# Performance work log

Hardware: AMD Instinct MI355X
Metric: run time of the kernel (lower is better)

The kernel has to match this reference:

```python
import jax, jax.numpy as jnp
import numpy as np

N = 100000
E = 1600000
NFEAT, NHID, NCLASS = 602, 128, 41
EPS = 1e-5


def _spmm(rows, cols, vals, h):
    # out[r] = sum_{e: rows[e]==r} vals[e] * h[cols[e]]
    return jax.ops.segment_sum(vals[:, None] * h[cols], rows, num_segments=N)


def _layernorm(h, g, b):
    mu = jnp.mean(h, axis=-1, keepdims=True)
    var = jnp.var(h, axis=-1, keepdims=True)
    return (h - mu) * jax.lax.rsqrt(var + EPS) * g + b


def setup_inputs() -> dict:
    key = jax.random.key(0)
    ks = jax.random.split(key, 12)
    x = jax.random.normal(ks[0], (N, NFEAT), dtype=jnp.float32)
    rows = jax.random.randint(ks[1], (3, E), 0, N, dtype=jnp.int32)
    cols = jax.random.randint(ks[2], (3, E), 0, N, dtype=jnp.int32)
    # normalized-adjacency-like edge weights (~1/avg_degree scale)
    vals = jax.random.uniform(ks[3], (3, E), dtype=jnp.float32) / 16.0
    W1 = jax.random.normal(ks[4], (NFEAT, NHID), dtype=jnp.float32) / np.sqrt(NFEAT)
    b1 = jnp.zeros((NHID,), dtype=jnp.float32)
    W2 = jax.random.normal(ks[5], (NHID, NHID), dtype=jnp.float32) / np.sqrt(NHID)
    b2 = jnp.zeros((NHID,), dtype=jnp.float32)
    W3 = jax.random.normal(ks[6], (NHID, NHID), dtype=jnp.float32) / np.sqrt(NHID)
    b3 = jnp.zeros((NHID,), dtype=jnp.float32)
    ln_g = jnp.ones((NHID,), dtype=jnp.float32)
    ln_b = jnp.zeros((NHID,), dtype=jnp.float32)
    Wout = jax.random.normal(ks[7], (NHID, NCLASS), dtype=jnp.float32) / np.sqrt(NHID)
    bout = jnp.zeros((NCLASS,), dtype=jnp.float32)
    return {"x": x, "rows": rows, "cols": cols, "vals": vals,
            "W1": W1, "b1": b1, "W2": W2, "b2": b2, "W3": W3, "b3": b3,
            "ln_g": ln_g, "ln_b": ln_b, "Wout": Wout, "bout": bout}


def reference(x, rows, cols, vals, W1, b1, W2, b2, W3, b3, ln_g, ln_b, Wout, bout):
    # gc1: spmm(adj0, x @ W1) + b1 -> shared LayerNorm -> ReLU (dropout = eval identity)
    h = _spmm(rows[0], cols[0], vals[0], x @ W1) + b1
    h = jax.nn.relu(_layernorm(h, ln_g, ln_b))
    # gc2 with adj1
    h = _spmm(rows[1], cols[1], vals[1], h @ W2) + b2
    h = jax.nn.relu(_layernorm(h, ln_g, ln_b))
    # gc3 with adj2
    h = _spmm(rows[2], cols[2], vals[2], h @ W3) + b3
    h = jax.nn.relu(_layernorm(h, ln_g, ln_b))
    logits = h @ Wout + bout
    return jax.nn.log_softmax(logits, axis=1)
```

## Files before the change

kernel.cpp:

```cpp
#include <hip/hip_runtime.h>
#include <cstddef>

#define N_NODES 100000
#define E_EDGES 1600000
#define NFEAT   602
#define NHID    128
#define NCLASS  41
#define LN_EPS  1e-5f

typedef __bf16 bf16x8 __attribute__((ext_vector_type(8)));
typedef float f32x4 __attribute__((ext_vector_type(4)));
typedef unsigned short ushort8 __attribute__((ext_vector_type(8)));
typedef int intx4 __attribute__((ext_vector_type(4)));
typedef float fltx4 __attribute__((ext_vector_type(4)));

__device__ inline float bflo(unsigned int u) {
    return __builtin_bit_cast(float, u << 16);
}
__device__ inline float bfhi(unsigned int u) {
    return __builtin_bit_cast(float, u & 0xFFFF0000u);
}
__device__ inline unsigned short f2bf(float f) {
    return __builtin_bit_cast(unsigned short, (__bf16)f);
}

#define NT1 19
#define NT2 4

__global__ __launch_bounds__(256) void k_prep_all(
    const float* __restrict__ W1, const float* __restrict__ W2,
    const float* __restrict__ W3, unsigned short* __restrict__ Wf1,
    unsigned short* __restrict__ Wf2, unsigned short* __restrict__ Wf3)
{
    const int wid = (blockIdx.x * 256 + threadIdx.x) >> 6;
    const int lane = threadIdx.x & 63;
    const float* W; unsigned short* Wf; int K; int lw;
    if (wid < NT1 * 8)            { W = W1; Wf = Wf1; K = NFEAT; lw = wid; }
    else if (wid < (NT1 + NT2) * 8) { W = W2; Wf = Wf2; K = NHID; lw = wid - NT1 * 8; }
    else if (wid < (NT1 + 2 * NT2) * 8) { W = W3; Wf = Wf3; K = NHID; lw = wid - (NT1 + NT2) * 8; }
    else return;
    const int t = lw >> 3, n = lw & 7;
    const int fr = lane & 15, kh = lane >> 4;
    const int c = n * 16 + fr;
    ushort8 v;
#pragma unroll
    for (int j = 0; j < 8; ++j) {
        int k = t * 32 + kh * 8 + j;
        float x = (k < K) ? W[(size_t)k * 128 + c] : 0.f;
        v[j] = f2bf(x);
    }
    *reinterpret_cast<ushort8*>(Wf + ((size_t)lw * 64 + lane) * 8) = v;
}

template<int KK, bool BF16A>
__global__ __launch_bounds__(512) void k_gemm_slab(
    const void* __restrict__ Ain, const unsigned short* __restrict__ Wfrag,
    unsigned short* __restrict__ C, int M)
{
    constexpr int NT = (KK + 31) / 32;
    constexpr int KPAD = ((KK + 7) / 8) * 8 + 8;
    __shared__ unsigned short As[64 * KPAD + 8];

    const int tid = threadIdx.x;
    const int row0 = blockIdx.x * 64;
    const int nrow = (M - row0 < 64) ? (M - row0) : 64;
    const int total = nrow * KK;

    if (!BF16A) {
        const float* A32 = (const float*)Ain + (size_t)row0 * KK;
        constexpr int totalFull = 64 * KK;
#pragma unroll 4
        for (int base = 0; base < totalFull; base += 2048) {
            int i = base + tid * 4;
            if (i < totalFull) {
                float4 v = make_float4(0.f, 0.f, 0.f, 0.f);
                if (i + 4 <= total) {
                    v = *reinterpret_cast<const float4*>(A32 + i);
                } else if (i < total) {
                    float tmp[4] = {0.f, 0.f, 0.f, 0.f};
#pragma unroll
                    for (int e = 0; e < 4; ++e) if (i + e < total) tmp[e] = A32[i + e];
                    v = make_float4(tmp[0], tmp[1], tmp[2], tmp[3]);
                }
                int row = i / KK;
                int col = i - row * KK;
                unsigned int d0 = (unsigned int)f2bf(v.x) | ((unsigned int)f2bf(v.y) << 16);
                unsigned int d1 = (unsigned int)f2bf(v.z) | ((unsigned int)f2bf(v.w) << 16);
                int a0 = row * KPAD + col;
                int a1 = (col == KK - 2) ? (row + 1) * KPAD : a0 + 2;
                *reinterpret_cast<unsigned int*>(&As[a0]) = d0;
                *reinterpret_cast<unsigned int*>(&As[a1]) = d1;
            }
        }
    } else {
        const unsigned short* A16 = (const unsigned short*)Ain + (size_t)row0 * KK;
        constexpr int totalFull = 64 * KK;
#pragma unroll
        for (int base = 0; base < totalFull; base += 4096) {
            int i = base + tid * 8;
            if (i < totalFull) {
                ushort8 v;
#pragma unroll
                for (int j = 0; j < 8; ++j) v[j] = 0;
                if (i + 8 <= total) v = *reinterpret_cast<const ushort8*>(A16 + i);
                int row = i / KK;
                int col = i - row * KK;
                *reinterpret_cast<ushort8*>(&As[row * KPAD + col]) = v;
            }
        }
    }
    __syncthreads();

    const int wv = tid >> 6, lane = tid & 63;
    const int fr = lane & 15, kh = lane >> 4;
    const int mfr = wv >> 1;
    const int ch = wv & 1;
    const unsigned short* abase = &As[(mfr * 16 + fr) * KPAD + kh * 8];
    const unsigned short* wbase = Wfrag + ((size_t)(ch * 4) * 64 + lane) * 8;

    f32x4 acc[4];
#pragma unroll
    for (int n = 0; n < 4; ++n) acc[n] = (f32x4)(0.f);

    bf16x8 bcur[4];
#pragma unroll
    for (int n = 0; n < 4; ++n)
        bcur[n] = __builtin_bit_cast(bf16x8,
            *reinterpret_cast<const ushort8*>(wbase + n * 512));

#pragma unroll
    for (int t = 0; t < NT; ++t) {
        bf16x8 bnext[4];
        if (t + 1 < NT) {
            const unsigned short* wp = wbase + (size_t)(t + 1) * 4096;
#pragma unroll
            for (int n = 0; n < 4; ++n)
                bnext[n] = __builtin_bit_cast(bf16x8,
                    *reinterpret_cast<const ushort8*>(wp + n * 512));
        }
        bf16x8 af = *reinterpret_cast<const bf16x8*>(abase + t * 32);
        if (KK % 32 != 0 && t == NT - 1) {
#pragma unroll
            for (int j = 0; j < 8; ++j)
                if (t * 32 + kh * 8 + j >= KK) af[j] = (__bf16)0.f;
        }
#pragma unroll
        for (int n = 0; n < 4; ++n)
            acc[n] = __builtin_amdgcn_mfma_f32_16x16x32_bf16(af, bcur[n], acc[n], 0, 0, 0);
#pragma unroll
        for (int n = 0; n < 4; ++n) bcur[n] = bnext[n];
    }

#pragma unroll
    for (int jj = 0; jj < 4; ++jj) {
        int cr = row0 + mfr * 16 + kh * 4 + jj;
        if (cr < M) {
#pragma unroll
            for (int n = 0; n < 4; ++n)
                C[(size_t)cr * NHID + ch * 64 + n * 16 + fr] = f2bf(acc[n][jj]);
        }
    }
}

__global__ void k_zero(int* __restrict__ p, int n)
{
    int i = blockIdx.x * blockDim.x + threadIdx.x;
    if (i < n) p[i] = 0;
}

#define NBUCK 8
#define RPB   12500
#define CAP_G 210000
#define DCAP  48

#define PCHUNK 3072
#define BPG    ((E_EDGES + PCHUNK - 1) / PCHUNK)
#define BCAP   512

__global__ __launch_bounds__(256) void k_partition(
    const int* __restrict__ rows, const int* __restrict__ cols,
    const float* __restrict__ vals,
    int* __restrict__ cntA, intx4* __restrict__ stage)
{
    __shared__ int br[NBUCK * BCAP];
    __shared__ int bc[NBUCK * BCAP];
    __shared__ int bv[NBUCK * BCAP];
    __shared__ int bcnt[NBUCK];
    __shared__ int bbase[NBUCK];

    const int g = blockIdx.x / BPG;
    const int chunk = blockIdx.x - g * BPG;
    const int e0 = chunk * PCHUNK;
    const int e1 = (e0 + PCHUNK < E_EDGES) ? (e0 + PCHUNK) : E_EDGES;
    const intx4* rg4 = reinterpret_cast<const intx4*>(rows + (size_t)g * E_EDGES);
    const intx4* cg4 = reinterpret_cast<const intx4*>(cols + (size_t)g * E_EDGES);
    const fltx4* vg4 = reinterpret_cast<const fltx4*>(vals + (size_t)g * E_EDGES);
    const int q0 = e0 >> 2, q1 = e1 >> 2;

    if (threadIdx.x < NBUCK) bcnt[threadIdx.x] = 0;
    __syncthreads();

    for (int i = q0 + (int)threadIdx.x; i < q1; i += 256) {
        intx4 r4 = __builtin_nontemporal_load(rg4 + i);
        intx4 c4 = __builtin_nontemporal_load(cg4 + i);
        fltx4 v4 = __builtin_nontemporal_load(vg4 + i);
#pragma unroll
        for (int u = 0; u < 4; ++u) {
            int r = r4[u];
            int c = c4[u];
            float v = v4[u];
            int b = r / RPB;
            int off = atomicAdd(&bcnt[b], 1);
            if (off < BCAP) {
                br[b * BCAP + off] = r;
                bc[b * BCAP + off] = c;
                bv[b * BCAP + off] = __builtin_bit_cast(int, v);
            } else {
                int p = atomicAdd(&cntA[g * NBUCK + b], 1);
                intx4 e;
                e.x = r; e.y = c; e.z = __builtin_bit_cast(int, v); e.w = 0;
                stage[(size_t)(g * NBUCK + b) * CAP_G + p] = e;
            }
        }
    }
    __syncthreads();

    if (threadIdx.x < NBUCK) {
        int n = bcnt[threadIdx.x];
        n = (n < BCAP) ? n : BCAP;
        bbase[threadIdx.x] = atomicAdd(&cntA[g * NBUCK + threadIdx.x], n);
        bcnt[threadIdx.x] = n;
    }
    __syncthreads();

#pragma unroll
    for (int b = 0; b < NBUCK; ++b) {
        int n = bcnt[b];
        int base = bbase[b];
        intx4* dst = stage + (size_t)(g * NBUCK + b) * CAP_G;
        for (int j = (int)threadIdx.x; j < n; j += 256) {
            intx4 e;
            e.x = br[b * BCAP + j];
            e.y = bc[b * BCAP + j];
            e.z = bv[b * BCAP + j];
            e.w = 0;
            dst[base + j] = e;
        }
    }
}

#define SLICES 256

__global__ __launch_bounds__(256) void k_scatter_l2(
    const intx4* __restrict__ stageG,
    const int* __restrict__ cntAG,
    int* __restrict__ fillG,
    int2* __restrict__ ecvG)
{
    const int b = blockIdx.x & 7;
    const int slice = blockIdx.x >> 3;
    const int n = cntAG[b];
    const intx4* sp = stageG + (size_t)b * CAP_G;
    for (int i = slice * 256 + (int)threadIdx.x; i < n; i += SLICES * 256) {
        intx4 e = __builtin_nontemporal_load(sp + i);
        int p = atomicAdd(&fillG[e.x], 1);
        if (p < DCAP)
            ecvG[(size_t)e.x * DCAP + p] = make_int2(e.y, e.z);
    }
}

__global__ __launch_bounds__(256) void k_spmm_ln(
    const unsigned short* __restrict__ Hin, const int* __restrict__ fillG,
    const int2* __restrict__ ecvG,
    const float* __restrict__ bias, const float* __restrict__ g,
    const float* __restrict__ bb, unsigned short* __restrict__ Hout)
{
    const int w = threadIdx.x >> 6;
    const int lane = threadIdx.x & 63;
    const int row = blockIdx.x * 4 + w;
    int cnt = fillG[row];
    cnt = (cnt < DCAP) ? cnt : DCAP;
    const int start = row * DCAP;
    const int end = start + cnt;
    const int2* ecv = ecvG;

    float a0 = 0.f, a1 = 0.f;
    int p = start;
    for (; p + 15 < end; p += 16) {
        int2 e[16];
        unsigned int h[16];
#pragma unroll
        for (int j = 0; j < 16; ++j) e[j] = ecv[p + j];
#pragma unroll
        for (int j = 0; j < 16; ++j)
            h[j] = *reinterpret_cast<const unsigned int*>(
                Hin + (size_t)e[j].x * NHID + 2 * lane);
#pragma unroll
        for (int j = 0; j < 16; ++j) {
            float v = __builtin_bit_cast(float, e[j].y);
            a0 += v * bflo(h[j]);
            a1 += v * bfhi(h[j]);
        }
    }
    for (; p + 7 < end; p += 8) {
        int2 e[8];
        unsigned int h[8];
#pragma unroll
        for (int j = 0; j < 8; ++j) e[j] = ecv[p + j];
#pragma unroll
        for (int j = 0; j < 8; ++j)
            h[j] = *reinterpret_cast<const unsigned int*>(
                Hin + (size_t)e[j].x * NHID + 2 * lane);
#pragma unroll
        for (int j = 0; j < 8; ++j) {
            float v = __builtin_bit_cast(float, e[j].y);
            a0 += v * bflo(h[j]);
            a1 += v * bfhi(h[j]);
        }
    }
    for (; p + 3 < end; p += 4) {
        int2 e[4];
        unsigned int h[4];
#pragma unroll
        for (int j = 0; j < 4; ++j) e[j] = ecv[p + j];
#pragma unroll
        for (int j = 0; j < 4; ++j)
            h[j] = *reinterpret_cast<const unsigned int*>(
                Hin + (size_t)e[j].x * NHID + 2 * lane);
#pragma unroll
        for (int j = 0; j < 4; ++j) {
            float v = __builtin_bit_cast(float, e[j].y);
            a0 += v * bflo(h[j]);
            a1 += v * bfhi(h[j]);
        }
    }
    for (; p < end; ++p) {
        int2 e = ecv[p];
        unsigned int h = *reinterpret_cast<const unsigned int*>(
            Hin + (size_t)e.x * NHID + 2 * lane);
        float v = __builtin_bit_cast(float, e.y);
        a0 += v * bflo(h);  a1 += v * bfhi(h);
    }
    {
        float2 bv = *reinterpret_cast<const float2*>(bias + 2 * lane);
        a0 += bv.x;  a1 += bv.y;
    }

    float sum = a0 + a1, sq = a0 * a0 + a1 * a1;
#pragma unroll
    for (int off = 32; off; off >>= 1) {
        sum += __shfl_xor(sum, off);
        sq  += __shfl_xor(sq, off);
    }
    float mu = sum * (1.f / 128.f);
    float var = sq * (1.f / 128.f) - mu * mu;
    float rs = rsqrtf(var + LN_EPS);
    float2 gv = *reinterpret_cast<const float2*>(g + 2 * lane);
    float2 bbv = *reinterpret_cast<const float2*>(bb + 2 * lane);
    float r0 = fmaxf((a0 - mu) * rs * gv.x + bbv.x, 0.f);
    float r1 = fmaxf((a1 - mu) * rs * gv.y + bbv.y, 0.f);
    unsigned int o = (unsigned int)f2bf(r0) | ((unsigned int)f2bf(r1) << 16);
    *reinterpret_cast<unsigned int*>(Hout + (size_t)row * NHID + 2 * lane) = o;
}

#define GOUT 2048
__global__ __launch_bounds__(256) void k_out(
    const unsigned short* __restrict__ H, const float* __restrict__ Wout,
    const float* __restrict__ bout, float* __restrict__ out)
{
    __shared__ float ws[NHID * NCLASS];
    __shared__ float bs[NCLASS];
    __shared__ float hrow[4][NHID];
    for (int i = threadIdx.x; i < NHID * NCLASS; i += 256) ws[i] = Wout[i];
    if (threadIdx.x < NCLASS) bs[threadIdx.x] = bout[threadIdx.x];
    __syncthreads();

    const int w = threadIdx.x >> 6;
    const int lane = threadIdx.x & 63;

    for (int rb = blockIdx.x; rb < N_NODES / 4; rb += GOUT) {
        const int row = rb * 4 + w;
        unsigned int hv = *reinterpret_cast<const unsigned int*>(
            H + (size_t)row * NHID + 2 * lane);
        hrow[w][2 * lane]     = bflo(hv);
        hrow[w][2 * lane + 1] = bfhi(hv);
        float acc = (lane < NCLASS) ? bs[lane] : 0.f;
        if (lane < NCLASS) {
#pragma unroll 8
            for (int k = 0; k < NHID; ++k) acc += hrow[w][k] * ws[k * NCLASS + lane];
        }
        float x = (lane < NCLASS) ? acc : -1e30f;
        float m = x;
#pragma unroll
        for (int off = 32; off; off >>= 1) m = fmaxf(m, __shfl_xor(m, off));
        float e = (lane < NCLASS) ? expf(x - m) : 0.f;
        float se = e;
#pragma unroll
        for (int off = 32; off; off >>= 1) se += __shfl_xor(se, off);
        if (lane < NCLASS) out[(size_t)row * NCLASS + lane] = x - m - logf(se);
    }
}

extern "C" void kernel_launch(void* const* d_in, const int* in_sizes, int n_in,
                              void* d_out, int out_size, void* d_ws, size_t ws_size,
                              hipStream_t stream)
{
    const float* x    = (const float*)d_in[0];
    const int*   rows = (const int*)  d_in[1];
    const int*   cols = (const int*)  d_in[2];
    const float* vals = (const float*)d_in[3];
    const float* W1   = (const float*)d_in[4];
    const float* b1   = (const float*)d_in[5];
    const float* W2   = (const float*)d_in[6];
    const float* b2   = (const float*)d_in[7];
    const float* W3   = (const float*)d_in[8];
    const float* b3   = (const float*)d_in[9];
    const float* ln_g = (const float*)d_in[10];
    const float* ln_b = (const float*)d_in[11];
    const float* Wout = (const float*)d_in[12];
    const float* bout = (const float*)d_in[13];
    float* out = (float*)d_out;

    unsigned short* HA16 = (unsigned short*)d_ws;
    unsigned short* HB16 = HA16 + (size_t)N_NODES * NHID;
    unsigned short* Wf1  = HB16 + (size_t)N_NODES * NHID;
    unsigned short* Wf2  = Wf1 + (size_t)NT1 * 4096;
    unsigned short* Wf3  = Wf2 + (size_t)NT2 * 4096;
    intx4* stage  = (intx4*)(Wf3 + (size_t)NT2 * 4096);
    int2* ecv3    = (int2*)(stage + (size_t)24 * CAP_G);
    int* fill3    = (int*)(ecv3 + (size_t)3 * N_NODES * DCAP);
    int* cntA     = fill3 + 3 * N_NODES;

    const int gGemm = (N_NODES + 63) / 64;
    const int gRow = N_NODES / 4;

    k_zero<<<(3 * N_NODES + 24 + 255) / 256, 256, 0, stream>>>(fill3, 3 * N_NODES + 24);
    k_partition<<<3 * BPG, 256, 0, stream>>>(rows, cols, vals, cntA, stage);
    for (int g = 0; g < 3; ++g) {
        k_scatter_l2<<<NBUCK * SLICES, 256, 0, stream>>>(
            stage + (size_t)g * NBUCK * CAP_G, cntA + g * NBUCK,
            fill3 + g * N_NODES, ecv3 + (size_t)g * N_NODES * DCAP);
    }

    k_prep_all<<<((NT1 + 2 * NT2) * 8 + 3) / 4, 256, 0, stream>>>(
        W1, W2, W3, Wf1, Wf2, Wf3);

    k_gemm_slab<NFEAT, false><<<gGemm, 512, 0, stream>>>(x, Wf1, HA16, N_NODES);
    k_spmm_ln<<<gRow, 256, 0, stream>>>(HA16, fill3, ecv3,
                                        b1, ln_g, ln_b, HB16);
    k_gemm_slab<NHID, true><<<gGemm, 512, 0, stream>>>(HB16, Wf2, HA16, N_NODES);
    k_spmm_ln<<<gRow, 256, 0, stream>>>(HA16, fill3 + N_NODES,
                                        ecv3 + (size_t)N_NODES * DCAP,
                                        b2, ln_g, ln_b, HB16);
    k_gemm_slab<NHID, true><<<gGemm, 512, 0, stream>>>(HB16, Wf3, HA16, N_NODES);
    k_spmm_ln<<<gRow, 256, 0, stream>>>(HA16, fill3 + 2 * N_NODES,
                                        ecv3 + (size_t)2 * N_NODES * DCAP,
                                        b3, ln_g, ln_b, HB16);
    k_out<<<GOUT, 256, 0, stream>>>(HB16, Wout, bout, out);
}
```

Measured before the change: 677.2 us.

## Overlap edge partitioning and scatter with GEMM and SpMM via role-split fused kernels

```diff
diff --git a/kernel.cpp b/kernel.cpp
--- a/kernel.cpp
+++ b/kernel.cpp
@@ -26,6 +26,16 @@
 
 #define NT1 19
 #define NT2 4
+
+#define NBUCK 8
+#define RPB   12500
+#define CAP_G 210000
+#define DCAP  48
+#define PCHUNK 3072
+#define BPG    ((E_EDGES + PCHUNK - 1) / PCHUNK)
+#define BCAP   512
+#define SLICES 256
+#define NSCAT  (NBUCK * SLICES)
 
 __global__ __launch_bounds__(256) void k_prep_all(
     const float* __restrict__ W1, const float* __restrict__ W2,
@@ -53,16 +63,14 @@
 }
 
 template<int KK, bool BF16A>
-__global__ __launch_bounds__(512) void k_gemm_slab(
+__device__ __forceinline__ void gemm_slab_body(
+    const int tid, const int row0, unsigned short* As,
     const void* __restrict__ Ain, const unsigned short* __restrict__ Wfrag,
     unsigned short* __restrict__ C, int M)
 {
     constexpr int NT = (KK + 31) / 32;
     constexpr int KPAD = ((KK + 7) / 8) * 8 + 8;
-    __shared__ unsigned short As[64 * KPAD + 8];
-
-    const int tid = threadIdx.x;
-    const int row0 = blockIdx.x * 64;
+
     const int nrow = (M - row0 < 64) ? (M - row0) : 64;
     const int total = nrow * KK;
 
@@ -162,34 +170,26 @@
     }
 }
 
-__global__ void k_zero(int* __restrict__ p, int n)
-{
-    int i = blockIdx.x * blockDim.x + threadIdx.x;
-    if (i < n) p[i] = 0;
-}
-
-#define NBUCK 8
-#define RPB   12500
-#define CAP_G 210000
-#define DCAP  48
-
-#define PCHUNK 3072
-#define BPG    ((E_EDGES + PCHUNK - 1) / PCHUNK)
-#define BCAP   512
-
-__global__ __launch_bounds__(256) void k_partition(
+template<int KK, bool BF16A>
+__global__ __launch_bounds__(512) void k_gemm_slab(
+    const void* __restrict__ Ain, const unsigned short* __restrict__ Wfrag,
+    unsigned short* __restrict__ C, int M)
+{
+    constexpr int KPAD = ((KK + 7) / 8) * 8 + 8;
+    __shared__ unsigned short As[64 * KPAD + 8];
+    gemm_slab_body<KK, BF16A>(threadIdx.x, blockIdx.x * 64, As, Ain, Wfrag, C, M);
+}
+
+template<int NTHR>
+__device__ __forceinline__ void partition_body(
+    const int tid, const int sub, int* br, int* bc, int* bv,
+    int* bcnt, int* bbase,
     const int* __restrict__ rows, const int* __restrict__ cols,
     const float* __restrict__ vals,
     int* __restrict__ cntA, intx4* __restrict__ stage)
 {
-    __shared__ int br[NBUCK * BCAP];
-    __shared__ int bc[NBUCK * BCAP];
-    __shared__ int bv[NBUCK * BCAP];
-    __shared__ int bcnt[NBUCK];
-    __shared__ int bbase[NBUCK];
-
-    const int g = blockIdx.x / BPG;
-    const int chunk = blockIdx.x - g * BPG;
+    const int g = sub / BPG;
+    const int chunk = sub - g * BPG;
     const int e0 = chunk * PCHUNK;
     const int e1 = (e0 + PCHUNK < E_EDGES) ? (e0 + PCHUNK) : E_EDGES;
     const intx4* rg4 = reinterpret_cast<const intx4*>(rows + (size_t)g * E_EDGES);
@@ -197,10 +197,10 @@
     const fltx4* vg4 = reinterpret_cast<const fltx4*>(vals + (size_t)g * E_EDGES);
     const int q0 = e0 >> 2, q1 = e1 >> 2;
 
-    if (threadIdx.x < NBUCK) bcnt[threadIdx.x] = 0;
+    if (tid < NBUCK) bcnt[tid] = 0;
     __syncthreads();
 
-    for (int i = q0 + (int)threadIdx.x; i < q1; i += 256) {
+    for (int i = q0 + tid; i < q1; i += NTHR) {
         intx4 r4 = __builtin_nontemporal_load(rg4 + i);
         intx4 c4 = __builtin_nontemporal_load(cg4 + i);
         fltx4 v4 = __builtin_nontemporal_load(vg4 + i);
@@ -225,11 +225,11 @@
     }
     __syncthreads();
 
-    if (threadIdx.x < NBUCK) {
-        int n = bcnt[threadIdx.x];
+    if (tid < NBUCK) {
+        int n = bcnt[tid];
         n = (n < BCAP) ? n : BCAP;
-        bbase[threadIdx.x] = atomicAdd(&cntA[g * NBUCK + threadIdx.x], n);
-        bcnt[threadIdx.x] = n;
+        bbase[tid] = atomicAdd(&cntA[g * NBUCK + tid], n);
+        bcnt[tid] = n;
     }
     __syncthreads();
 
@@ -238,7 +238,7 @@
         int n = bcnt[b];
         int base = bbase[b];
         intx4* dst = stage + (size_t)(g * NBUCK + b) * CAP_G;
-        for (int j = (int)threadIdx.x; j < n; j += 256) {
+        for (int j = tid; j < n; j += NTHR) {
             intx4 e;
             e.x = br[b * BCAP + j];
             e.y = bc[b * BCAP + j];
@@ -249,16 +249,33 @@
     }
 }
 
-#define SLICES 256
-
-__global__ __launch_bounds__(256) void k_scatter_l2(
-    const intx4* __restrict__ stageG,
-    const int* __restrict__ cntAG,
-    int* __restrict__ fillG,
-    int2* __restrict__ ecvG)
-{
-    const int b = blockIdx.x & 7;
-    const int slice = blockIdx.x >> 3;
+#define F1_SMEM 78880
+__global__ __launch_bounds__(512) void k_f1(
+    const float* __restrict__ x, const unsigned short* __restrict__ Wf1,
+    unsigned short* __restrict__ HA16,
+    const int* __restrict__ rows, const int* __restrict__ cols,
+    const float* __restrict__ vals,
+    int* __restrict__ cntA, intx4* __restrict__ stage)
+{
+    __shared__ __align__(16) char smem[F1_SMEM];
+    const int role = blockIdx.x & 1;
+    const int sub = blockIdx.x >> 1;
+    if (role == 0) {
+        gemm_slab_body<NFEAT, false>(threadIdx.x, sub * 64,
+                                     (unsigned short*)smem, x, Wf1, HA16, N_NODES);
+    } else {
+        int* br = (int*)smem;
+        partition_body<512>(threadIdx.x, sub, br, br + 4096, br + 8192,
+                            br + 12288, br + 12296, rows, cols, vals, cntA, stage);
+    }
+}
+
+__device__ __forceinline__ void scatter_body(
+    int bid, const intx4* __restrict__ stageG, const int* __restrict__ cntAG,
+    int* __restrict__ fillG, int2* __restrict__ ecvG)
+{
+    const int b = bid & 7;
+    const int slice = bid >> 3;
     const int n = cntAG[b];
     const intx4* sp = stageG + (size_t)b * CAP_G;
     for (int i = slice * 256 + (int)threadIdx.x; i < n; i += SLICES * 256) {
@@ -269,20 +286,26 @@
     }
 }
 
-__global__ __launch_bounds__(256) void k_spmm_ln(
-    const unsigned short* __restrict__ Hin, const int* __restrict__ fillG,
-    const int2* __restrict__ ecvG,
+__global__ __launch_bounds__(256) void k_scatter_l2(
+    const intx4* __restrict__ stageG, const int* __restrict__ cntAG,
+    int* __restrict__ fillG, int2* __restrict__ ecvG)
+{
+    scatter_body(blockIdx.x, stageG, cntAG, fillG, ecvG);
+}
+
+__device__ __forceinline__ void spmm_body(
+    int sub, const unsigned short* __restrict__ Hin,
+    const int* __restrict__ fillG, const int2* __restrict__ ecv,
     const float* __restrict__ bias, const float* __restrict__ g,
     const float* __restrict__ bb, unsigned short* __restrict__ Hout)
 {
     const int w = threadIdx.x >> 6;
     const int lane = threadIdx.x & 63;
-    const int row = blockIdx.x * 4 + w;
+    const int row = sub * 4 + w;
     int cnt = fillG[row];
     cnt = (cnt < DCAP) ? cnt : DCAP;
     const int start = row * DCAP;
     const int end = start + cnt;
-    const int2* ecv = ecvG;
 
     float a0 = 0.f, a1 = 0.f;
     int p = start;
@@ -361,6 +384,35 @@
     float r1 = fmaxf((a1 - mu) * rs * gv.y + bbv.y, 0.f);
     unsigned int o = (unsigned int)f2bf(r0) | ((unsigned int)f2bf(r1) << 16);
     *reinterpret_cast<unsigned int*>(Hout + (size_t)row * NHID + 2 * lane) = o;
+}
+
+__global__ __launch_bounds__(256) void k_spmm_ln(
+    const unsigned short* __restrict__ Hin, const int* __restrict__ fillG,
+    const int2* __restrict__ ecvG,
+    const float* __restrict__ bias, const float* __restrict__ g,
+    const float* __restrict__ bb, unsigned short* __restrict__ Hout)
+{
+    spmm_body(blockIdx.x, Hin, fillG, ecvG, bias, g, bb, Hout);
+}
+
+__global__ __launch_bounds__(256) void k_spmm_scat(
+    const unsigned short* __restrict__ Hin, const int* __restrict__ fillR,
+    const int2* __restrict__ ecvR,
+    const float* __restrict__ bias, const float* __restrict__ g,
+    const float* __restrict__ bb, unsigned short* __restrict__ Hout,
+    const intx4* __restrict__ stageS, const int* __restrict__ cntAS,
+    int* __restrict__ fillS, int2* __restrict__ ecvS)
+{
+    if (blockIdx.x < NSCAT)
+        scatter_body(blockIdx.x, stageS, cntAS, fillS, ecvS);
+    else
+        spmm_body(blockIdx.x - NSCAT, Hin, fillR, ecvR, bias, g, bb, Hout);
+}
+
+__global__ void k_zero(int* __restrict__ p, int n)
+{
+    int i = blockIdx.x * blockDim.x + threadIdx.x;
+    if (i < n) p[i] = 0;
 }
 
 #define GOUT 2048
@@ -435,24 +487,27 @@
     const int gRow = N_NODES / 4;
 
     k_zero<<<(3 * N_NODES + 24 + 255) / 256, 256, 0, stream>>>(fill3, 3 * N_NODES + 24);
-    k_partition<<<3 * BPG, 256, 0, stream>>>(rows, cols, vals, cntA, stage);
-    for (int g = 0; g < 3; ++g) {
-        k_scatter_l2<<<NBUCK * SLICES, 256, 0, stream>>>(
-            stage + (size_t)g * NBUCK * CAP_G, cntA + g * NBUCK,
-            fill3 + g * N_NODES, ecv3 + (size_t)g * N_NODES * DCAP);
-    }
-
     k_prep_all<<<((NT1 + 2 * NT2) * 8 + 3) / 4, 256, 0, stream>>>(
         W1, W2, W3, Wf1, Wf2, Wf3);
 
-    k_gemm_slab<NFEAT, false><<<gGemm, 512, 0, stream>>>(x, Wf1, HA16, N_NODES);
-    k_spmm_ln<<<gRow, 256, 0, stream>>>(HA16, fill3, ecv3,
-                                        b1, ln_g, ln_b, HB16);
+    k_f1<<<2 * gGemm, 512, 0, stream>>>(x, Wf1, HA16, rows, cols, vals, cntA, stage);
+
+    k_scatter_l2<<<NSCAT, 256, 0, stream>>>(stage, cntA, fill3, ecv3);
+
+    k_spmm_scat<<<NSCAT + gRow, 256, 0, stream>>>(
+        HA16, fill3, ecv3, b1, ln_g, ln_b, HB16,
+        stage + (size_t)NBUCK * CAP_G, cntA + NBUCK,
+        fill3 + N_NODES, ecv3 + (size_t)N_NODES * DCAP);
+
     k_gemm_slab<NHID, true><<<gGemm, 512, 0, stream>>>(HB16, Wf2, HA16, N_NODES);
-    k_spmm_ln<<<gRow, 256, 0, stream>>>(HA16, fill3 + N_NODES,
-                                        ecv3 + (size_t)N_NODES * DCAP,
-                                        b2, ln_g, ln_b, HB16);
+
+    k_spmm_scat<<<NSCAT + gRow, 256, 0, stream>>>(
+        HA16, fill3 + N_NODES, ecv3 + (size_t)N_NODES * DCAP, b2, ln_g, ln_b, HB16,
+        stage + (size_t)2 * NBUCK * CAP_G, cntA + 2 * NBUCK,
+        fill3 + 2 * N_NODES, ecv3 + (size_t)2 * N_NODES * DCAP);
+
     k_gemm_slab<NHID, true><<<gGemm, 512, 0, stream>>>(HB16, Wf3, HA16, N_NODES);
+
     k_spmm_ln<<<gRow, 256, 0, stream>>>(HA16, fill3 + 2 * N_NODES,
                                         ecv3 + (size_t)2 * N_NODES * DCAP,
                                         b3, ln_g, ln_b, HB16);
```

Result: slower. 717.7 us (+6.0%).
